# Optimization experiments

Measured on AMD Instinct MI355X. Metric: run time of the kernel, lower is better.

The kernel has to match this reference:

```python
import jax, jax.numpy as jnp
import numpy as np

N = 50000   # total nodes
E = 800000  # total edges (avg degree 16)
D = 128     # input_dim == hidden_dim
G = 256     # graphs in batch
C = 16      # output classes
L = 5       # num_layers
BN_EPS = 1e-5


def setup_inputs() -> dict:
    key = jax.random.key(0)
    ks = jax.random.split(key, 8)
    s = 1.0 / np.sqrt(D)
    return {
        "x": jax.random.normal(ks[0], (N, D), dtype=jnp.float32),
        "eps": jnp.zeros((L - 1,), dtype=jnp.float32),
        "W1": jax.random.normal(ks[1], (L - 1, D, D), dtype=jnp.float32) * s,
        "b1": jnp.zeros((L - 1, D), dtype=jnp.float32),
        "g1": jnp.ones((L - 1, D), dtype=jnp.float32),
        "beta1": jnp.zeros((L - 1, D), dtype=jnp.float32),
        "W2": jax.random.normal(ks[2], (L - 1, D, D), dtype=jnp.float32) * s,
        "b2": jnp.zeros((L - 1, D), dtype=jnp.float32),
        "g2": jnp.ones((L - 1, D), dtype=jnp.float32),
        "beta2": jnp.zeros((L - 1, D), dtype=jnp.float32),
        "Wp": jax.random.normal(ks[3], (L, D, C), dtype=jnp.float32) * s,
        "bp": jnp.zeros((L, C), dtype=jnp.float32),
        "edge_src": jax.random.randint(ks[4], (E,), 0, N),
        "edge_dst": jax.random.randint(ks[5], (E,), 0, N),
        "graph_ids": jnp.sort(jax.random.randint(ks[6], (N,), 0, G)),
    }


def _bn(x, g, b):
    # BatchNorm1d in training mode: biased batch statistics over the node axis
    m = jnp.mean(x, axis=0)
    v = jnp.mean(jnp.square(x - m), axis=0)
    return g * (x - m) * jax.lax.rsqrt(v + BN_EPS) + b


def reference(x, eps, W1, b1, g1, beta1, W2, b2, g2, beta2, Wp, bp,
              edge_src, edge_dst, graph_ids):
    hidden_representations = [x]
    h = x
    for l in range(L - 1):
        # spmm(adj, h): gather neighbor features along edges, scatter-add to dst
        pooled = jax.ops.segment_sum(h[edge_src], edge_dst, num_segments=N)
        pooled = pooled + (1.0 + eps[l]) * h  # learn_eps branch
        # MLP (num_mlp_layers=2): Linear+BN+ReLU, then Linear
        z = jax.nn.relu(_bn(pooled @ W1[l] + b1[l], g1[l], beta1[l]))
        z = z @ W2[l] + b2[l]
        # outer BN + ReLU
        h = jax.nn.relu(_bn(z, g2[l], beta2[l]))
        hidden_representations.append(h)

    out = jnp.zeros((G, C), dtype=x.dtype)
    for l, hl in enumerate(hidden_representations):
        # graph_pool spmm: sum-pool node features per graph
        pooled_h = jax.ops.segment_sum(hl, graph_ids, num_segments=G)
        out = out + pooled_h @ Wp[l] + bp[l]  # dropout p=0 -> identity
    return out
```

## Files before the change

### kernel.cpp

```cpp
#include <hip/hip_runtime.h>

#define N_NODES  50000
#define N_EDGES  800000
#define DIM      128
#define N_GRAPHS 256
#define N_CLASSES 16
#define N_LAYERS 5
#define BN_EPS   1e-5f

#define GEMM_BM 64
#define LDSP 136

typedef short bf16x8 __attribute__((ext_vector_type(8)));
typedef float f32x4  __attribute__((ext_vector_type(4)));

__device__ __forceinline__ float bf2f(unsigned short u) {
    unsigned int x = ((unsigned int)u) << 16;
    return __builtin_bit_cast(float, x);
}
__device__ __forceinline__ unsigned short f2bf(float f) {
    unsigned int x = __builtin_bit_cast(unsigned int, f);
    x += 0x7fffu + ((x >> 16) & 1u);
    return (unsigned short)(x >> 16);
}
__device__ __forceinline__ float lo16(unsigned int v) { return bf2f((unsigned short)(v & 0xffffu)); }
__device__ __forceinline__ float hi16(unsigned int v) { return bf2f((unsigned short)(v >> 16)); }
__device__ __forceinline__ unsigned int pack16(float a, float b) {
    return (unsigned int)f2bf(a) | ((unsigned int)f2bf(b) << 16);
}


__global__ void degbound_kernel(const int* __restrict__ dst, int* __restrict__ deg,
                                const int* __restrict__ gid, int* __restrict__ gptr) {
    int i = blockIdx.x * blockDim.x + threadIdx.x;
    if (i < N_EDGES) atomicAdd(&deg[dst[i]], 1);
    if (i < N_NODES) {
        int cur = gid[i];
        int prev = (i == 0) ? -1 : gid[i - 1];
        for (int g = prev + 1; g <= cur; ++g) gptr[g] = i;
        if (i == N_NODES - 1)
            for (int g = cur + 1; g <= N_GRAPHS; ++g) gptr[g] = N_NODES;
    }
}

__global__ void fill_csr_kernel(const int* __restrict__ src, const int* __restrict__ dst,
                                int* __restrict__ cursor, int* __restrict__ csr, int e_count) {
    int e = blockIdx.x * blockDim.x + threadIdx.x;
    if (e < e_count) {
        int d = dst[e];
        int p = atomicAdd(&cursor[d], 1);
        csr[p] = src[e];
    }
}

__global__ void zrow_kernel(unsigned short* __restrict__ a, unsigned short* __restrict__ b) {
    int t = threadIdx.x;
    uint2 z = make_uint2(0u, 0u);
    if (t < 32) ((uint2*)(a + (size_t)N_NODES * DIM))[t] = z;
    else        ((uint2*)(b + (size_t)N_NODES * DIM))[t - 32] = z;
}


__global__ __launch_bounds__(1024) void scan_part_kernel(const int* __restrict__ in,
                                                         int* __restrict__ part, int n) {
    __shared__ int red[16];
    int tid = threadIdx.x;
    int i = blockIdx.x * 1024 + tid;
    int v = (i < n) ? in[i] : 0;
#pragma unroll
    for (int d = 1; d < 64; d <<= 1) v += __shfl_xor(v, d, 64);
    int lane = tid & 63, w = tid >> 6;
    if (lane == 0) red[w] = v;
    __syncthreads();
    if (tid == 0) {
        int s = 0;
#pragma unroll
        for (int k = 0; k < 16; ++k) s += red[k];
        part[blockIdx.x] = s;
    }
}

__global__ void scan_mid_kernel(int* __restrict__ part, int nb,
                                int* __restrict__ total_out, int total_idx) {
    int lane = threadIdx.x;
    int orig = (lane < nb) ? part[lane] : 0;
    int v = orig;
#pragma unroll
    for (int d = 1; d < 64; d <<= 1) {
        int t = __shfl_up(v, d, 64);
        if (lane >= d) v += t;
    }
    if (lane < nb) part[lane] = v - orig;
    if (lane == 63) total_out[total_idx] = v;
}

__global__ __launch_bounds__(1024) void scan_final_kernel(const int* __restrict__ in,
                                                          const int* __restrict__ part,
                                                          int* __restrict__ rowptr,
                                                          int* __restrict__ cursor, int n) {
    __shared__ int woff[16];
    int tid = threadIdx.x;
    int i = blockIdx.x * 1024 + tid;
    int v = (i < n) ? in[i] : 0;
    int lane = tid & 63, w = tid >> 6;
    int x = v;
#pragma unroll
    for (int d = 1; d < 64; d <<= 1) {
        int t = __shfl_up(x, d, 64);
        if (lane >= d) x += t;
    }
    if (lane == 63) woff[w] = x;
    __syncthreads();
    if (tid == 0) {
        int s = 0;
#pragma unroll
        for (int k = 0; k < 16; ++k) { int t = woff[k]; woff[k] = s; s += t; }
    }
    __syncthreads();
    int excl = part[blockIdx.x] + woff[w] + x - v;
    if (i < n) { rowptr[i] = excl; cursor[i] = excl; }
}


#define CVT_F2B_BLOCKS 2048
#define CVT_W_BLOCKS   64

__global__ __launch_bounds__(256) void convert_kernel(
    const float* __restrict__ x, unsigned short* __restrict__ xb,
    const float* __restrict__ W1, const float* __restrict__ W2,
    unsigned short* __restrict__ Wt1, unsigned short* __restrict__ Wt2,
    const int* __restrict__ gptr, float* __restrict__ pool0)
{
    __shared__ float red[DIM];
    int b = blockIdx.x, tid = threadIdx.x;
    if (b < N_GRAPHS) {
        int c = tid & 127;
        int half = tid >> 7;
        int beg = gptr[b], end = gptr[b + 1];
        float acc = 0.f;
        for (int n = beg + half; n < end; n += 2) acc += x[(size_t)n * DIM + c];
        if (half == 1) red[c] = acc;
        __syncthreads();
        if (half == 0) pool0[(size_t)b * DIM + c] = acc + red[c];
    } else if (b < N_GRAPHS + CVT_F2B_BLOCKS) {
        const int total_data = N_NODES * DIM / 4;
        const int total = (N_NODES + 1) * DIM / 4;
        const int stride = CVT_F2B_BLOCKS * 256;
        for (int i = (b - N_GRAPHS) * 256 + tid; i < total; i += stride) {
            uint2 o = make_uint2(0u, 0u);
            if (i < total_data) {
                float4 v = ((const float4*)x)[i];
                o = make_uint2(pack16(v.x, v.y), pack16(v.z, v.w));
            }
            ((uint2*)xb)[i] = o;
        }
    } else {
        const int total = (N_LAYERS - 1) * DIM * DIM;
        const int stride = CVT_W_BLOCKS * 256;
        for (int t = (b - N_GRAPHS - CVT_F2B_BLOCKS) * 256 + tid; t < total; t += stride) {
            int m = t >> 14;
            int k = (t & 16383) >> 7;
            int c = t & 127;
            size_t dstp = ((size_t)m << 14) + (size_t)c * DIM + k;
            Wt1[dstp] = f2bf(W1[t]);
            Wt2[dstp] = f2bf(W2[t]);
        }
    }
}


__device__ __forceinline__ void gemm_core8(
    unsigned short (*As)[LDSP], const unsigned short* __restrict__ Wt,
    unsigned short* __restrict__ Z, float* __restrict__ colsum, float* __restrict__ colsumsq,
    int nrows, int row0, int tid)
{
    int wid = tid >> 6, lane = tid & 63;
    int mq = wid & 3, ch = wid >> 2;
    int m0 = mq * 16;
    int lrow = lane & 15;
    int lk = (lane >> 4) * 8;

    f32x4 acc[4];
#pragma unroll
    for (int n = 0; n < 4; ++n) acc[n] = (f32x4){0.f, 0.f, 0.f, 0.f};

#pragma unroll
    for (int kk = 0; kk < 4; ++kk) {
        int k0 = kk * 32;
        bf16x8 a = *(const bf16x8*)&As[m0 + lrow][k0 + lk];
#pragma unroll
        for (int n = 0; n < 4; ++n) {
            bf16x8 b = *(const bf16x8*)(Wt + (size_t)(ch * 64 + n * 16 + lrow) * DIM + k0 + lk);
            acc[n] = __builtin_amdgcn_mfma_f32_16x16x32_bf16(a, b, acc[n], 0, 0, 0);
        }
    }

    int r0 = row0 + m0 + (lane >> 4) * 4;
    float sarr[4], qarr[4];
#pragma unroll
    for (int n = 0; n < 4; ++n) {
        int col = ch * 64 + n * 16 + lrow;
        float s = 0.f, q = 0.f;
#pragma unroll
        for (int j = 0; j < 4; ++j) {
            float v = acc[n][j];
            int row = r0 + j;
            if (row < nrows) Z[(size_t)row * DIM + col] = f2bf(v);
            s += v; q += v * v;
        }
        s += __shfl_xor(s, 16); q += __shfl_xor(q, 16);
        s += __shfl_xor(s, 32); q += __shfl_xor(q, 32);
        sarr[n] = s; qarr[n] = q;
    }

    __syncthreads();
    float* red = (float*)&As[0][0];
    if (lane < 16) {
#pragma unroll
        for (int n = 0; n < 4; ++n) {
            int col = ch * 64 + n * 16 + lrow;
            red[wid * 256 + col]       = sarr[n];
            red[wid * 256 + 128 + col] = qarr[n];
        }
    }
    __syncthreads();
    if (tid < 128) {
        int col = tid;
        int base = (col >> 6) * 4 * 256;
        float ts = red[base + col] + red[base + 256 + col]
                 + red[base + 512 + col] + red[base + 768 + col];
        float tq = red[base + 128 + col] + red[base + 384 + col]
                 + red[base + 640 + col] + red[base + 896 + col];
        atomicAdd(&colsum[col], ts);
        atomicAdd(&colsumsq[col], tq);
    }
}


__global__ __launch_bounds__(512) void gemmA_kernel(
    const unsigned short* __restrict__ h, const int* __restrict__ rowptr,
    const int* __restrict__ csr, const float* __restrict__ epsArr, int l,
    const unsigned short* __restrict__ Wt, unsigned short* __restrict__ Z,
    float* __restrict__ stats, int nrows)
{
    __shared__ __attribute__((aligned(16))) unsigned short As[GEMM_BM][LDSP];
    int tid = threadIdx.x;
    int row0 = blockIdx.x * GEMM_BM;
    int wid = tid >> 6, lane = tid & 63;
    int nsel = lane >> 5, esub = (lane >> 4) & 1, chunk = lane & 15;
    float ep = 1.0f + epsArr[l];

    for (int t = 0; t < 4; ++t) {
        int node = row0 + wid * 8 + t * 2 + nsel;
        bool valid = node < nrows;
        int beg = 0, end = 0;
        if (valid) { beg = rowptr[node]; end = rowptr[node + 1]; }

        int sidx[8];
#pragma unroll
        for (int k = 0; k < 8; ++k) {
            int ee = beg + esub + 2 * k;
            int ec = (ee < N_EDGES) ? ee : (N_EDGES - 1);
            int sv = csr[ec];
            sidx[k] = (valid && ee < end) ? sv : N_NODES;
        }
        bf16x8 v[8];
#pragma unroll
        for (int k = 0; k < 8; ++k)
            v[k] = *(const bf16x8*)(h + (size_t)sidx[k] * DIM + chunk * 8);

        float a8[8];
#pragma unroll
        for (int j = 0; j < 8; ++j) a8[j] = 0.f;
#pragma unroll
        for (int k = 0; k < 8; ++k)
#pragma unroll
            for (int j = 0; j < 8; ++j)
                a8[j] += bf2f((unsigned short)v[k][j]);

        if (valid) {
            for (int e = beg + 16 + esub; e < end; e += 2) {
                int sv = csr[e];
                bf16x8 vv = *(const bf16x8*)(h + (size_t)sv * DIM + chunk * 8);
#pragma unroll
                for (int j = 0; j < 8; ++j) a8[j] += bf2f((unsigned short)vv[j]);
            }
        }

#pragma unroll
        for (int j = 0; j < 8; ++j) a8[j] += __shfl_xor(a8[j], 16);

        if (valid) {
            bf16x8 hv = *(const bf16x8*)(h + (size_t)node * DIM + chunk * 8);
#pragma unroll
            for (int j = 0; j < 8; ++j) a8[j] += ep * bf2f((unsigned short)hv[j]);
        }

        if (esub == 0) {
            bf16x8 o;
#pragma unroll
            for (int j = 0; j < 8; ++j) o[j] = (short)f2bf(a8[j]);
            *(bf16x8*)&As[wid * 8 + t * 2 + nsel][chunk * 8] = o;
        }
    }
    __syncthreads();
    gemm_core8(As, Wt, Z, stats, stats + 128, nrows, row0, tid);
}


__global__ __launch_bounds__(512) void gemmB_kernel(
    const unsigned short* __restrict__ Zin, const float* __restrict__ statsIn,
    const float* __restrict__ g, const float* __restrict__ beta,
    const unsigned short* __restrict__ Wt, unsigned short* __restrict__ Zout,
    float* __restrict__ statsOut, int nrows)
{
    __shared__ __attribute__((aligned(16))) unsigned short As[GEMM_BM][LDSP];
    __shared__ float abn[DIM], shbn[DIM];
    int tid = threadIdx.x;
    int row0 = blockIdx.x * GEMM_BM;

    if (tid < DIM) {
        const float invN = 1.0f / (float)N_NODES;
        float m = statsIn[tid] * invN;
        float var = statsIn[128 + tid] * invN - m * m;
        float s = g[tid] * rsqrtf(var + BN_EPS);
        abn[tid] = s;
        shbn[tid] = beta[tid] - s * m;
    }
    __syncthreads();

#pragma unroll
    for (int it = 0; it < 2; ++it) {
        int c = tid + it * 512;
        int r = c >> 4, kc = c & 15;
        bf16x8 o = {0, 0, 0, 0, 0, 0, 0, 0};
        if (row0 + r < nrows) {
            bf16x8 v = *(const bf16x8*)(Zin + (size_t)(row0 + r) * DIM + kc * 8);
#pragma unroll
            for (int cc = 0; cc < 8; ++cc) {
                int col = kc * 8 + cc;
                float f = bf2f((unsigned short)v[cc]);
                f = fmaxf(fmaf(abn[col], f, shbn[col]), 0.f);
                o[cc] = (short)f2bf(f);
            }
        }
        *(bf16x8*)&As[r][kc * 8] = o;
    }
    __syncthreads();
    gemm_core8(As, Wt, Zout, statsOut, statsOut + 128, nrows, row0, tid);
}


__global__ __launch_bounds__(256) void bnpool_kernel(
    const unsigned short* __restrict__ Zin, const float* __restrict__ stats,
    const float* __restrict__ g, const float* __restrict__ beta,
    const int* __restrict__ gid, unsigned short* __restrict__ hout,
    float* __restrict__ pooled, int nrows)
{
    __shared__ float abn[DIM], shbn[DIM];
    int tid = threadIdx.x;
    if (tid < DIM) {
        const float invN = 1.0f / (float)N_NODES;
        float m = stats[tid] * invN;
        float var = stats[128 + tid] * invN - m * m;
        float s = g[tid] * rsqrtf(var + BN_EPS);
        abn[tid] = s;
        shbn[tid] = beta[tid] - s * m;
    }
    __syncthreads();

    int row0 = blockIdx.x * GEMM_BM;
    int lane = tid & 63, w = tid >> 6;
    int c0 = lane * 2;
    float a0 = abn[c0], a1 = abn[c0 + 1], s0 = shbn[c0], s1 = shbn[c0 + 1];
    const unsigned int* Z2 = (const unsigned int*)Zin;
    unsigned int* H2 = (unsigned int*)hout;

    float px = 0.f, py = 0.f;
    int gcur = -1;
    for (int i = 0; i < 16; ++i) {
        int r = row0 + w * 16 + i;
        if (r >= nrows) break;
        int gg = gid[r];
        if (gg != gcur) {
            if (gcur >= 0) {
                atomicAdd(&pooled[(size_t)gcur * DIM + c0], px);
                atomicAdd(&pooled[(size_t)gcur * DIM + c0 + 1], py);
            }
            gcur = gg; px = 0.f; py = 0.f;
        }
        unsigned int v = Z2[(size_t)r * 64 + lane];
        float f0 = fmaxf(fmaf(a0, lo16(v), s0), 0.f);
        float f1 = fmaxf(fmaf(a1, hi16(v), s1), 0.f);
        unsigned int o = pack16(f0, f1);
        H2[(size_t)r * 64 + lane] = o;
        px += lo16(o);
        py += hi16(o);
    }
    if (gcur >= 0) {
        atomicAdd(&pooled[(size_t)gcur * DIM + c0], px);
        atomicAdd(&pooled[(size_t)gcur * DIM + c0 + 1], py);
    }
}


__global__ __launch_bounds__(256) void final_kernel(
    const float* __restrict__ pooledH, const float* __restrict__ Wp,
    const float* __restrict__ bp, float* __restrict__ outp)
{
    int t = blockIdx.x * blockDim.x + threadIdx.x;
    if (t >= N_GRAPHS * N_CLASSES) return;
    int g = t >> 4, c = t & 15;
    float acc = 0.f;
    for (int l = 0; l < N_LAYERS; ++l) {
        const float* ph = pooledH + ((size_t)l * N_GRAPHS + g) * DIM;
        const float* w = Wp + (size_t)l * DIM * N_CLASSES + c;
        float a = 0.f;
        for (int k = 0; k < DIM; ++k) a = fmaf(ph[k], w[k * N_CLASSES], a);
        acc += a + bp[l * N_CLASSES + c];
    }
    outp[t] = acc;
}


extern "C" void kernel_launch(void* const* d_in, const int* in_sizes, int n_in,
                              void* d_out, int out_size, void* d_ws, size_t ws_size,
                              hipStream_t stream) {
    const float* x     = (const float*)d_in[0];
    const float* eps   = (const float*)d_in[1];
    const float* W1    = (const float*)d_in[2];
    const float* g1    = (const float*)d_in[4];
    const float* beta1 = (const float*)d_in[5];
    const float* W2    = (const float*)d_in[6];
    const float* g2    = (const float*)d_in[8];
    const float* beta2 = (const float*)d_in[9];
    const float* Wp    = (const float*)d_in[10];
    const float* bp    = (const float*)d_in[11];
    const int*   esrc  = (const int*)d_in[12];
    const int*   edst  = (const int*)d_in[13];
    const int*   gid   = (const int*)d_in[14];
    float* outp = (float*)d_out;

    char* ws = (char*)d_ws;
    size_t off = 0;
    auto alloc = [&](size_t bytes) {
        char* p = ws + off;
        off = (off + bytes + 255) & ~(size_t)255;
        return p;
    };
    unsigned short* xb  = (unsigned short*)alloc((size_t)(N_NODES + 1) * DIM * 2);
    unsigned short* B0  = (unsigned short*)alloc((size_t)(N_NODES + 1) * DIM * 2);
    unsigned short* B1  = (unsigned short*)alloc((size_t)(N_NODES + 1) * DIM * 2);
    unsigned short* ZB  = (unsigned short*)alloc((size_t)N_NODES * DIM * 2);
    unsigned short* Z2B = (unsigned short*)alloc((size_t)N_NODES * DIM * 2);
    unsigned short* Wt1 = (unsigned short*)alloc((size_t)(N_LAYERS - 1) * DIM * DIM * 2);
    unsigned short* Wt2 = (unsigned short*)alloc((size_t)(N_LAYERS - 1) * DIM * DIM * 2);
    int*   csr     = (int*)alloc((size_t)N_EDGES * 4);
    int*   deg     = (int*)alloc((N_NODES + 1) * 4);
    int*   rowptr  = (int*)alloc((N_NODES + 1) * 4);
    int*   cursor  = (int*)alloc((N_NODES + 1) * 4);
    int*   part    = (int*)alloc(64 * 4);
    int*   growptr = (int*)alloc(300 * 4);
    float* stats   = (float*)alloc(8 * 256 * 4);
    float* pooledH = (float*)alloc((size_t)N_LAYERS * N_GRAPHS * DIM * 4);

    hipMemsetAsync(deg, 0, N_NODES * 4, stream);
    hipMemsetAsync(stats, 0, 8 * 256 * 4, stream);
    hipMemsetAsync(pooledH, 0, (size_t)N_LAYERS * N_GRAPHS * DIM * 4, stream);

    const int nsb = (N_NODES + 1023) / 1024;
    degbound_kernel<<<(N_EDGES + 255) / 256, 256, 0, stream>>>(edst, deg, gid, growptr);
    scan_part_kernel<<<nsb, 1024, 0, stream>>>(deg, part, N_NODES);
    scan_mid_kernel<<<1, 64, 0, stream>>>(part, nsb, rowptr, N_NODES);
    scan_final_kernel<<<nsb, 1024, 0, stream>>>(deg, part, rowptr, cursor, N_NODES);
    fill_csr_kernel<<<(N_EDGES + 255) / 256, 256, 0, stream>>>(esrc, edst, cursor, csr, N_EDGES);
    zrow_kernel<<<1, 64, 0, stream>>>(B0, B1);

    convert_kernel<<<N_GRAPHS + CVT_F2B_BLOCKS + CVT_W_BLOCKS, 256, 0, stream>>>(
        x, xb, W1, W2, Wt1, Wt2, growptr, pooledH);

    const int ngrid = (N_NODES + GEMM_BM - 1) / GEMM_BM;
    const unsigned short* hb = xb;
    unsigned short* nb = B0;
    for (int l = 0; l < N_LAYERS - 1; ++l) {
        float* statsA = stats + (size_t)(2 * l) * 256;
        float* statsB = stats + (size_t)(2 * l + 1) * 256;
        gemmA_kernel<<<ngrid, 512, 0, stream>>>(
            hb, rowptr, csr, eps, l, Wt1 + (size_t)l * DIM * DIM, ZB, statsA, N_NODES);
        gemmB_kernel<<<ngrid, 512, 0, stream>>>(
            ZB, statsA, g1 + (size_t)l * DIM, beta1 + (size_t)l * DIM,
            Wt2 + (size_t)l * DIM * DIM, Z2B, statsB, N_NODES);
        bnpool_kernel<<<ngrid, 256, 0, stream>>>(
            Z2B, statsB, g2 + (size_t)l * DIM, beta2 + (size_t)l * DIM,
            gid, nb, pooledH + (size_t)(l + 1) * N_GRAPHS * DIM, N_NODES);

        hb = nb;
        nb = (nb == B0) ? B1 : B0;
    }

    final_kernel<<<(N_GRAPHS * N_CLASSES + 255) / 256, 256, 0, stream>>>(pooledH, Wp, bp, outp);
}
```

Measured before the change: 700.9 us.

## Stage block CSR edges in LDS and gather one node per wave

```diff
diff --git a/kernel.cpp b/kernel.cpp
--- a/kernel.cpp
+++ b/kernel.cpp
@@ -10,6 +10,7 @@
 
 #define GEMM_BM 64
 #define LDSP 136
+#define ECAP 2048
 
 typedef short bf16x8 __attribute__((ext_vector_type(8)));
 typedef float f32x4  __attribute__((ext_vector_type(4)));
@@ -51,13 +52,6 @@
         int p = atomicAdd(&cursor[d], 1);
         csr[p] = src[e];
     }
-}
-
-__global__ void zrow_kernel(unsigned short* __restrict__ a, unsigned short* __restrict__ b) {
-    int t = threadIdx.x;
-    uint2 z = make_uint2(0u, 0u);
-    if (t < 32) ((uint2*)(a + (size_t)N_NODES * DIM))[t] = z;
-    else        ((uint2*)(b + (size_t)N_NODES * DIM))[t - 32] = z;
 }
 
 
@@ -143,16 +137,11 @@
         __syncthreads();
         if (half == 0) pool0[(size_t)b * DIM + c] = acc + red[c];
     } else if (b < N_GRAPHS + CVT_F2B_BLOCKS) {
-        const int total_data = N_NODES * DIM / 4;
-        const int total = (N_NODES + 1) * DIM / 4;
+        const int total = N_NODES * DIM / 4;
         const int stride = CVT_F2B_BLOCKS * 256;
         for (int i = (b - N_GRAPHS) * 256 + tid; i < total; i += stride) {
-            uint2 o = make_uint2(0u, 0u);
-            if (i < total_data) {
-                float4 v = ((const float4*)x)[i];
-                o = make_uint2(pack16(v.x, v.y), pack16(v.z, v.w));
-            }
-            ((uint2*)xb)[i] = o;
+            float4 v = ((const float4*)x)[i];
+            ((uint2*)xb)[i] = make_uint2(pack16(v.x, v.y), pack16(v.z, v.w));
         }
     } else {
         const int total = (N_LAYERS - 1) * DIM * DIM;
@@ -237,6 +226,47 @@
 }
 
 
+#define GATHER_TIERS(IDX)                                                        \
+    {                                                                            \
+        int e = beg;                                                             \
+        for (; e + 16 <= end; e += 16) {                                         \
+            int s0 = IDX(e + sub);                                               \
+            int s1 = IDX(e + 4 + sub);                                           \
+            int s2 = IDX(e + 8 + sub);                                           \
+            int s3 = IDX(e + 12 + sub);                                          \
+            bf16x8 v0 = *(const bf16x8*)(h + (size_t)s0 * DIM + chunk * 8);      \
+            bf16x8 v1 = *(const bf16x8*)(h + (size_t)s1 * DIM + chunk * 8);      \
+            bf16x8 v2 = *(const bf16x8*)(h + (size_t)s2 * DIM + chunk * 8);      \
+            bf16x8 v3 = *(const bf16x8*)(h + (size_t)s3 * DIM + chunk * 8);      \
+            _Pragma("unroll")                                                    \
+            for (int j = 0; j < 8; ++j)                                          \
+                a8[j] += (bf2f((unsigned short)v0[j]) + bf2f((unsigned short)v1[j])) \
+                       + (bf2f((unsigned short)v2[j]) + bf2f((unsigned short)v3[j])); \
+        }                                                                        \
+        for (; e + 8 <= end; e += 8) {                                           \
+            int s0 = IDX(e + sub);                                               \
+            int s1 = IDX(e + 4 + sub);                                           \
+            bf16x8 v0 = *(const bf16x8*)(h + (size_t)s0 * DIM + chunk * 8);      \
+            bf16x8 v1 = *(const bf16x8*)(h + (size_t)s1 * DIM + chunk * 8);      \
+            _Pragma("unroll")                                                    \
+            for (int j = 0; j < 8; ++j)                                          \
+                a8[j] += bf2f((unsigned short)v0[j]) + bf2f((unsigned short)v1[j]); \
+        }                                                                        \
+        for (; e + 4 <= end; e += 4) {                                           \
+            int s0 = IDX(e + sub);                                               \
+            bf16x8 v0 = *(const bf16x8*)(h + (size_t)s0 * DIM + chunk * 8);      \
+            _Pragma("unroll")                                                    \
+            for (int j = 0; j < 8; ++j) a8[j] += bf2f((unsigned short)v0[j]);    \
+        }                                                                        \
+        int rmn = end - e;                                                       \
+        if (sub < rmn) {                                                         \
+            int s0 = IDX(e + sub);                                               \
+            bf16x8 v0 = *(const bf16x8*)(h + (size_t)s0 * DIM + chunk * 8);      \
+            _Pragma("unroll")                                                    \
+            for (int j = 0; j < 8; ++j) a8[j] += bf2f((unsigned short)v0[j]);    \
+        }                                                                        \
+    }
+
 __global__ __launch_bounds__(512) void gemmA_kernel(
     const unsigned short* __restrict__ h, const int* __restrict__ rowptr,
     const int* __restrict__ csr, const float* __restrict__ epsArr, int l,
@@ -244,63 +274,59 @@
     float* __restrict__ stats, int nrows)
 {
     __shared__ __attribute__((aligned(16))) unsigned short As[GEMM_BM][LDSP];
+    __shared__ int Es[ECAP];
+    __shared__ int Rp[GEMM_BM + 1];
     int tid = threadIdx.x;
     int row0 = blockIdx.x * GEMM_BM;
     int wid = tid >> 6, lane = tid & 63;
-    int nsel = lane >> 5, esub = (lane >> 4) & 1, chunk = lane & 15;
+    int sub = lane >> 4, chunk = lane & 15;
     float ep = 1.0f + epsArr[l];
 
-    for (int t = 0; t < 4; ++t) {
-        int node = row0 + wid * 8 + t * 2 + nsel;
-        bool valid = node < nrows;
-        int beg = 0, end = 0;
-        if (valid) { beg = rowptr[node]; end = rowptr[node + 1]; }
-
-        int sidx[8];
-#pragma unroll
-        for (int k = 0; k < 8; ++k) {
-            int ee = beg + esub + 2 * k;
-            int ec = (ee < N_EDGES) ? ee : (N_EDGES - 1);
-            int sv = csr[ec];
-            sidx[k] = (valid && ee < end) ? sv : N_NODES;
-        }
-        bf16x8 v[8];
-#pragma unroll
-        for (int k = 0; k < 8; ++k)
-            v[k] = *(const bf16x8*)(h + (size_t)sidx[k] * DIM + chunk * 8);
-
+    int top = row0 + GEMM_BM; if (top > nrows) top = nrows;
+    int e_base = rowptr[row0];
+    int e_top  = rowptr[top];
+    int ecount = e_top - e_base;
+    if (tid <= GEMM_BM) {
+        int nidx = row0 + tid;
+        Rp[tid] = rowptr[nidx <= nrows ? nidx : nrows] - e_base;
+    }
+    int ecap = ecount < ECAP ? ecount : ECAP;
+    for (int i = tid; i < ecap; i += 512) Es[i] = csr[e_base + i];
+    __syncthreads();
+
+    const int* csr_g = csr + e_base;
+
+    for (int i = 0; i < 8; ++i) {
+        int li = wid * 8 + i;
+        int node = row0 + li;
         float a8[8];
 #pragma unroll
         for (int j = 0; j < 8; ++j) a8[j] = 0.f;
-#pragma unroll
-        for (int k = 0; k < 8; ++k)
-#pragma unroll
-            for (int j = 0; j < 8; ++j)
-                a8[j] += bf2f((unsigned short)v[k][j]);
-
-        if (valid) {
-            for (int e = beg + 16 + esub; e < end; e += 2) {
-                int sv = csr[e];
-                bf16x8 vv = *(const bf16x8*)(h + (size_t)sv * DIM + chunk * 8);
-#pragma unroll
-                for (int j = 0; j < 8; ++j) a8[j] += bf2f((unsigned short)vv[j]);
+        if (node < nrows) {
+            int beg = Rp[li], end = Rp[li + 1];
+            if (end <= ECAP) {
+#define IDX_L(E) Es[E]
+                GATHER_TIERS(IDX_L)
+#undef IDX_L
+            } else {
+#define IDX_G(E) csr_g[E]
+                GATHER_TIERS(IDX_G)
+#undef IDX_G
             }
-        }
-
-#pragma unroll
-        for (int j = 0; j < 8; ++j) a8[j] += __shfl_xor(a8[j], 16);
-
-        if (valid) {
+#pragma unroll
+            for (int j = 0; j < 8; ++j) {
+                a8[j] += __shfl_xor(a8[j], 16);
+                a8[j] += __shfl_xor(a8[j], 32);
+            }
             bf16x8 hv = *(const bf16x8*)(h + (size_t)node * DIM + chunk * 8);
 #pragma unroll
             for (int j = 0; j < 8; ++j) a8[j] += ep * bf2f((unsigned short)hv[j]);
         }
-
-        if (esub == 0) {
+        if (sub == 0) {
             bf16x8 o;
 #pragma unroll
             for (int j = 0; j < 8; ++j) o[j] = (short)f2bf(a8[j]);
-            *(bf16x8*)&As[wid * 8 + t * 2 + nsel][chunk * 8] = o;
+            *(bf16x8*)&As[wid * 8 + i][chunk * 8] = o;
         }
     }
     __syncthreads();
@@ -448,9 +474,9 @@
         off = (off + bytes + 255) & ~(size_t)255;
         return p;
     };
-    unsigned short* xb  = (unsigned short*)alloc((size_t)(N_NODES + 1) * DIM * 2);
-    unsigned short* B0  = (unsigned short*)alloc((size_t)(N_NODES + 1) * DIM * 2);
-    unsigned short* B1  = (unsigned short*)alloc((size_t)(N_NODES + 1) * DIM * 2);
+    unsigned short* xb  = (unsigned short*)alloc((size_t)N_NODES * DIM * 2);
+    unsigned short* B0  = (unsigned short*)alloc((size_t)N_NODES * DIM * 2);
+    unsigned short* B1  = (unsigned short*)alloc((size_t)N_NODES * DIM * 2);
     unsigned short* ZB  = (unsigned short*)alloc((size_t)N_NODES * DIM * 2);
     unsigned short* Z2B = (unsigned short*)alloc((size_t)N_NODES * DIM * 2);
     unsigned short* Wt1 = (unsigned short*)alloc((size_t)(N_LAYERS - 1) * DIM * DIM * 2);
@@ -474,7 +500,6 @@
     scan_mid_kernel<<<1, 64, 0, stream>>>(part, nsb, rowptr, N_NODES);
     scan_final_kernel<<<nsb, 1024, 0, stream>>>(deg, part, rowptr, cursor, N_NODES);
     fill_csr_kernel<<<(N_EDGES + 255) / 256, 256, 0, stream>>>(esrc, edst, cursor, csr, N_EDGES);
-    zrow_kernel<<<1, 64, 0, stream>>>(B0, B1);
 
     convert_kernel<<<N_GRAPHS + CVT_F2B_BLOCKS + CVT_W_BLOCKS, 256, 0, stream>>>(
         x, xb, W1, W2, Wt1, Wt2, growptr, pooledH);
```

After: 653.8 us. 6.7% less time.
